# Kernel tuning notes

Measured on AMD Instinct MI355X. Metric: run time of the kernel, lower is better.

The kernel has to match this reference:

```python
import jax, jax.numpy as jnp
import numpy as np

N = 12288
IN_DIM = 128
OUT_DIM = 128
LR_SLOPE = 0.01
NEG_INF = -9e16


def setup_inputs() -> dict:
    key = jax.random.key(0)
    k1, k2, k3, k4 = jax.random.split(key, 4)
    emb_mat = jax.random.normal(k1, (N, IN_DIM), dtype=jnp.float32)
    adj_mat = jax.random.randint(k2, (N, N), 0, 2, dtype=jnp.int32)
    # xavier-normal-ish init for params
    W = jax.random.normal(k3, (OUT_DIM, IN_DIM), dtype=jnp.float32) * (2.0 / (IN_DIM + OUT_DIM)) ** 0.5
    a = jax.random.normal(k4, (2 * OUT_DIM, 1), dtype=jnp.float32) * (2.0 / (2 * OUT_DIM + 1)) ** 0.5
    return {"emb_mat": emb_mat, "adj_mat": adj_mat, "W": W, "a": a}


def reference(emb_mat, adj_mat, W, a):
    out_dim = W.shape[0]
    e_new = emb_mat @ W.T                       # [N, D_out]
    a1 = a[:out_dim, :]                         # [D_out, 1]
    a2 = a[out_dim:, :]                         # [D_out, 1]
    source_scores = e_new @ a1                  # [N, 1]
    target_scores = e_new @ a2                  # [N, 1]
    e = source_scores + target_scores.T         # [N, N] outer sum
    e = jax.nn.leaky_relu(e, negative_slope=LR_SLOPE)
    e = jnp.where(adj_mat > 0, e, NEG_INF)
    attention = jax.nn.softmax(e, axis=-1)      # [N, N]
    e_transf = attention @ e_new                # [N, D_out]
    return jax.nn.relu(e_transf)
```

## Files before the change

### kernel.cpp

```cpp
#include <hip/hip_runtime.h>


#define NN 12288
#define DIM 128
#define CSPLIT 8
#define COLS_PER (NN / CSPLIT)
#define BK 32
#define NCHUNK (COLS_PER / BK)
#define LOG2E 1.4426950408889634f

typedef __bf16 bf16x8 __attribute__((ext_vector_type(8)));
typedef float f32x4 __attribute__((ext_vector_type(4)));

__device__ __forceinline__ void gl_lds16(const __bf16* g, __bf16* l) {
  __builtin_amdgcn_global_load_lds(
      (const __attribute__((address_space(1))) void*)g,
      (__attribute__((address_space(3))) void*)l, 16, 0, 0);
}

__global__ __launch_bounds__(256) void k1_gemm(const float* __restrict__ emb,
                                               const float* __restrict__ W,
                                               const float* __restrict__ a,
                                               __bf16* __restrict__ Vt,
                                               float* __restrict__ s,
                                               float* __restrict__ t) {
  const int lane = threadIdx.x & 63;
  const int wave = threadIdx.x >> 6;
  const int m = lane & 15;
  const int quad = lane >> 4;
  const int row0 = blockIdx.x * 64 + wave * 16;

  f32x4 acc[8];
#pragma unroll
  for (int nb = 0; nb < 8; nb++) acc[nb] = (f32x4){0.f, 0.f, 0.f, 0.f};

#pragma unroll
  for (int ks = 0; ks < 4; ks++) {
    const int k0 = ks * 32 + quad * 8;
    const float* ep = emb + (size_t)(row0 + m) * DIM + k0;
    float4 lo = *(const float4*)ep;
    float4 hi = *(const float4*)(ep + 4);
    bf16x8 af = {(__bf16)lo.x, (__bf16)lo.y, (__bf16)lo.z, (__bf16)lo.w,
                 (__bf16)hi.x, (__bf16)hi.y, (__bf16)hi.z, (__bf16)hi.w};
#pragma unroll
    for (int nb = 0; nb < 8; nb++) {
      const float* wp = W + (size_t)(nb * 16 + m) * DIM + k0;
      float4 wlo = *(const float4*)wp;
      float4 whi = *(const float4*)(wp + 4);
      bf16x8 bf = {(__bf16)wlo.x, (__bf16)wlo.y, (__bf16)wlo.z, (__bf16)wlo.w,
                   (__bf16)whi.x, (__bf16)whi.y, (__bf16)whi.z, (__bf16)whi.w};
      acc[nb] = __builtin_amdgcn_mfma_f32_16x16x32_bf16(af, bf, acc[nb], 0, 0, 0);
    }
  }

  float a1v[8], a2v[8];
#pragma unroll
  for (int nb = 0; nb < 8; nb++) {
    a1v[nb] = a[nb * 16 + m];
    a2v[nb] = a[DIM + nb * 16 + m];
  }
#pragma unroll
  for (int r = 0; r < 4; r++) {
    const int gr = row0 + quad * 4 + r;
    float ps = 0.f, pt = 0.f;
#pragma unroll
    for (int nb = 0; nb < 8; nb++) {
      float e = acc[nb][r];
      ps += e * a1v[nb];
      pt += e * a2v[nb];
      Vt[(size_t)(nb * 16 + m) * NN + gr] = (__bf16)e;
    }
    ps += __shfl_xor(ps, 1); ps += __shfl_xor(ps, 2);
    ps += __shfl_xor(ps, 4); ps += __shfl_xor(ps, 8);
    pt += __shfl_xor(pt, 1); pt += __shfl_xor(pt, 2);
    pt += __shfl_xor(pt, 4); pt += __shfl_xor(pt, 8);
    if (m == 0) { s[gr] = ps * LOG2E; t[gr] = pt * LOG2E; }
  }
}

__global__ __launch_bounds__(256) void ktmax(const float* __restrict__ t,
                                             float* __restrict__ tmax) {
  __shared__ float red[4];
  const float4* t4 = (const float4*)t;
  float mx = -3.0e38f;
#pragma unroll
  for (int i = 0; i < NN / 4 / 256; i++) {
    float4 v = t4[i * 256 + threadIdx.x];
    mx = fmaxf(mx, fmaxf(fmaxf(v.x, v.y), fmaxf(v.z, v.w)));
  }
#pragma unroll
  for (int off = 1; off < 64; off <<= 1) mx = fmaxf(mx, __shfl_xor(mx, off));
  if ((threadIdx.x & 63) == 0) red[threadIdx.x >> 6] = mx;
  __syncthreads();
  if (threadIdx.x == 0)
    *tmax = fmaxf(fmaxf(red[0], red[1]), fmaxf(red[2], red[3]));
}

#define PELS(P, AA0, AA1, T0, T1, SS, MM, LL)                                   \
  {                                                                             \
    float v0 = SS + T0.x, v1 = SS + T0.y, v2 = SS + T0.z, v3 = SS + T0.w;       \
    float v4 = SS + T1.x, v5 = SS + T1.y, v6 = SS + T1.z, v7 = SS + T1.w;       \
    float e0 = (AA0.x != 0) ? __builtin_amdgcn_exp2f(fmaxf(v0, 0.01f * v0) - MM) : 0.f; \
    float e1 = (AA0.y != 0) ? __builtin_amdgcn_exp2f(fmaxf(v1, 0.01f * v1) - MM) : 0.f; \
    float e2 = (AA0.z != 0) ? __builtin_amdgcn_exp2f(fmaxf(v2, 0.01f * v2) - MM) : 0.f; \
    float e3 = (AA0.w != 0) ? __builtin_amdgcn_exp2f(fmaxf(v3, 0.01f * v3) - MM) : 0.f; \
    float e4 = (AA1.x != 0) ? __builtin_amdgcn_exp2f(fmaxf(v4, 0.01f * v4) - MM) : 0.f; \
    float e5 = (AA1.y != 0) ? __builtin_amdgcn_exp2f(fmaxf(v5, 0.01f * v5) - MM) : 0.f; \
    float e6 = (AA1.z != 0) ? __builtin_amdgcn_exp2f(fmaxf(v6, 0.01f * v6) - MM) : 0.f; \
    float e7 = (AA1.w != 0) ? __builtin_amdgcn_exp2f(fmaxf(v7, 0.01f * v7) - MM) : 0.f; \
    LL += ((e0 + e1) + (e2 + e3)) + ((e4 + e5) + (e6 + e7));                    \
    P[0] = (__bf16)e0; P[1] = (__bf16)e1; P[2] = (__bf16)e2; P[3] = (__bf16)e3; \
    P[4] = (__bf16)e4; P[5] = (__bf16)e5; P[6] = (__bf16)e6; P[7] = (__bf16)e7; \
  }

#define FETCH(cc, A0A, A1A, A0B, A1B, T0, T1)                                   \
  {                                                                             \
    const int off = (cc) * BK;                                                  \
    A0A = *(const int4*)(abase + off); A1A = *(const int4*)(abase + off + 4);   \
    A0B = *(const int4*)(bbase + off); A1B = *(const int4*)(bbase + off + 4);   \
    T0 = *(const float4*)(tbase + off); T1 = *(const float4*)(tbase + off + 4); \
  }

#define DMA2(cc)                                                                \
  {                                                                             \
    __bf16* d = &vtb[(cc) & 3][dst0];                                           \
    gl_lds16(vsrc0 + (size_t)(cc) * BK, d);                                     \
    gl_lds16(vsrc1 + (size_t)(cc) * BK, d + 512);                               \
  }

#define COMPUTE(cc, A0A, A1A, A0B, A1B, T0, T1)                                 \
  {                                                                             \
    const __bf16* vb = &vtb[(cc) & 3][vread];                                   \
    bf16x8 pA, pB;                                                              \
    PELS(pA, A0A, A1A, T0, T1, sA, mA, lA)                                      \
    PELS(pB, A0B, A1B, T0, T1, sB, mB, lB)                                      \
    _Pragma("unroll")                                                           \
    for (int nb = 0; nb < 8; nb++) {                                            \
      bf16x8 bv = *(const bf16x8*)(vb + nb * 512);                              \
      accA[nb] = __builtin_amdgcn_mfma_f32_16x16x32_bf16(pA, bv, accA[nb], 0, 0, 0); \
      accB[nb] = __builtin_amdgcn_mfma_f32_16x16x32_bf16(pB, bv, accB[nb], 0, 0, 0); \
    }                                                                           \
  }

__global__ __launch_bounds__(256, 3) void k2_attn(const int* __restrict__ adj,
                                                  const __bf16* __restrict__ Vt,
                                                  const float* __restrict__ sK,
                                                  const float* __restrict__ tK,
                                                  const float* __restrict__ tmaxp,
                                                  float* __restrict__ part,
                                                  float* __restrict__ lpart) {
  __shared__ __attribute__((aligned(16))) __bf16 vtb[4][4096];

  const int tid = threadIdx.x;
  const int lane = tid & 63;
  const int wave = tid >> 6;
  const int m = lane & 15;
  const int quad = lane >> 4;
  const int row0 = blockIdx.x * 128;
  const int cs = blockIdx.y;
  const int col0 = cs * COLS_PER;
  const int rowA = row0 + wave * 32 + m;
  const int rowB = rowA + 16;

  const float TmaxK = *tmaxp;
  const float sA = sK[rowA], sB = sK[rowB];
  const float uA = sA + TmaxK, uB = sB + TmaxK;
  const float mA = fmaxf(uA, 0.01f * uA);
  const float mB = fmaxf(uB, 0.01f * uB);

  const int p0 = wave * 128 + lane;
  const int r0d = p0 >> 2;
  const int cg0 = (p0 & 3) ^ ((r0d >> 1) & 3);
  const __bf16* vsrc0 = Vt + (size_t)r0d * NN + col0 + cg0 * 8;
  const __bf16* vsrc1 = vsrc0 + (size_t)16 * NN;
  const int dst0 = wave * 1024;
  const int vread = (m * 4 + (quad ^ ((m >> 1) & 3))) * 8;

  const int* abase = adj + (size_t)rowA * NN + col0 + quad * 8;
  const int* bbase = adj + (size_t)rowB * NN + col0 + quad * 8;
  const float* tbase = tK + col0 + quad * 8;

  f32x4 accA[8], accB[8];
#pragma unroll
  for (int nb = 0; nb < 8; nb++) {
    accA[nb] = (f32x4){0.f, 0.f, 0.f, 0.f};
    accB[nb] = (f32x4){0.f, 0.f, 0.f, 0.f};
  }
  float lA = 0.f, lB = 0.f;

  int4 xA0, xA1, xB0, xB1; float4 xT0, xT1;
  int4 yA0, yA1, yB0, yB1; float4 yT0, yT1;

  DMA2(0);
  DMA2(1);
  FETCH(0, xA0, xA1, xB0, xB1, xT0, xT1);
  asm volatile("s_waitcnt vmcnt(0)" ::: "memory");
  __builtin_amdgcn_s_barrier();

  for (int c = 0; c < NCHUNK; c += 2) {
    if (c + 2 < NCHUNK) DMA2(c + 2);
    FETCH(c + 1, yA0, yA1, yB0, yB1, yT0, yT1);
    COMPUTE(c, xA0, xA1, xB0, xB1, xT0, xT1);
    asm volatile("s_waitcnt vmcnt(4)" ::: "memory");
    __builtin_amdgcn_s_barrier();

    if (c + 3 < NCHUNK) DMA2(c + 3);
    if (c + 2 < NCHUNK) FETCH(c + 2, xA0, xA1, xB0, xB1, xT0, xT1);
    COMPUTE(c + 1, yA0, yA1, yB0, yB1, yT0, yT1);
    if (c + 2 < NCHUNK) {
      asm volatile("s_waitcnt vmcnt(4)" ::: "memory");
      __builtin_amdgcn_s_barrier();
    }
  }

  lA += __shfl_xor(lA, 16); lA += __shfl_xor(lA, 32);
  lB += __shfl_xor(lB, 16); lB += __shfl_xor(lB, 32);
  if (quad == 0) {
    lpart[(size_t)cs * NN + rowA] = lA;
    lpart[(size_t)cs * NN + rowB] = lB;
  }

  float* po = part + ((size_t)cs * NN + row0 + wave * 32) * DIM;
#pragma unroll
  for (int nb = 0; nb < 8; nb++) {
#pragma unroll
    for (int r = 0; r < 4; r++) {
      po[(size_t)(quad * 4 + r) * DIM + nb * 16 + m] = accA[nb][r];
      po[(size_t)(16 + quad * 4 + r) * DIM + nb * 16 + m] = accB[nb][r];
    }
  }
}

__global__ __launch_bounds__(256) void k3_fin(const float* __restrict__ part,
                                              const float* __restrict__ lpart,
                                              float* __restrict__ out) {
  __shared__ float li[8];
  const int base = blockIdx.x * 256;
  const int idx = base + (int)threadIdx.x;
  if (threadIdx.x < 8) {
    const int r = (base >> 5) + (int)threadIdx.x;
    float l = 0.f;
#pragma unroll
    for (int c2 = 0; c2 < CSPLIT; c2++) l += lpart[(size_t)c2 * NN + r];
    li[threadIdx.x] = 1.0f / l;
  }
  const float4* p4 = (const float4*)part;
  float4 acc = p4[idx];
#pragma unroll
  for (int c2 = 1; c2 < CSPLIT; c2++) {
    float4 v = p4[(size_t)c2 * (NN * DIM / 4) + idx];
    acc.x += v.x; acc.y += v.y; acc.z += v.z; acc.w += v.w;
  }
  __syncthreads();
  const float liv = li[threadIdx.x >> 5];
  float4 o;
  o.x = fmaxf(acc.x * liv, 0.f);
  o.y = fmaxf(acc.y * liv, 0.f);
  o.z = fmaxf(acc.z * liv, 0.f);
  o.w = fmaxf(acc.w * liv, 0.f);
  ((float4*)out)[idx] = o;
}

extern "C" void kernel_launch(void* const* d_in, const int* in_sizes, int n_in,
                              void* d_out, int out_size, void* d_ws, size_t ws_size,
                              hipStream_t stream) {
  (void)in_sizes; (void)n_in; (void)out_size; (void)ws_size;
  const float* emb = (const float*)d_in[0];
  const int* adj = (const int*)d_in[1];
  const float* W = (const float*)d_in[2];
  const float* a = (const float*)d_in[3];
  float* out = (float*)d_out;

  char* ws = (char*)d_ws;
  __bf16* Vt = (__bf16*)ws;
  float* s = (float*)(ws + 3145728);
  float* t = (float*)(ws + 3194880);
  float* lpart = (float*)(ws + 3244032);
  float* tmax = (float*)(ws + 3686400);
  float* part = (float*)(ws + 3686656);

  k1_gemm<<<NN / 64, 256, 0, stream>>>(emb, W, a, Vt, s, t);
  ktmax<<<1, 256, 0, stream>>>(t, tmax);
  dim3 g2(NN / 128, CSPLIT);
  k2_attn<<<g2, 256, 0, stream>>>(adj, Vt, s, t, tmax, part, lpart);
  k3_fin<<<NN * DIM / 4 / 256, 256, 0, stream>>>(part, lpart, out);
}
```

Baseline: 832.8 us.

## Load V operand directly from global memory instead of staging through LDS

Removes the LDS staging of the transposed V tiles (global_load_lds DMA, swizzled layout, barriers) and has each wave read its bf16 V fragments straight from global/L2 inside the MFMA loop. The t-score loads move into the compute step. The grid is flattened to 1D with the column split as the fastest index, so blocks sharing a column slice of V run close together and can hit in cache. This removes barrier and LDS overhead and the 3-block occupancy hint, but adds redundant per-wave global loads of V with long stride and makes latency hiding depend on the compiler.

After: 957.9 us. 15.0% more time.

```diff
diff --git a/kernel.cpp b/kernel.cpp
--- a/kernel.cpp
+++ b/kernel.cpp
@@ -11,12 +11,6 @@
 
 typedef __bf16 bf16x8 __attribute__((ext_vector_type(8)));
 typedef float f32x4 __attribute__((ext_vector_type(4)));
-
-__device__ __forceinline__ void gl_lds16(const __bf16* g, __bf16* l) {
-  __builtin_amdgcn_global_load_lds(
-      (const __attribute__((address_space(1))) void*)g,
-      (__attribute__((address_space(3))) void*)l, 16, 0, 0);
-}
 
 __global__ __launch_bounds__(256) void k1_gemm(const float* __restrict__ emb,
                                                const float* __restrict__ W,
@@ -113,51 +107,46 @@
     P[4] = (__bf16)e4; P[5] = (__bf16)e5; P[6] = (__bf16)e6; P[7] = (__bf16)e7; \
   }
 
-#define FETCH(cc, A0A, A1A, A0B, A1B, T0, T1)                                   \
+#define FETCH(cc, A0A, A1A, A0B, A1B)                                           \
   {                                                                             \
     const int off = (cc) * BK;                                                  \
     A0A = *(const int4*)(abase + off); A1A = *(const int4*)(abase + off + 4);   \
     A0B = *(const int4*)(bbase + off); A1B = *(const int4*)(bbase + off + 4);   \
-    T0 = *(const float4*)(tbase + off); T1 = *(const float4*)(tbase + off + 4); \
-  }
-
-#define DMA2(cc)                                                                \
+  }
+
+#define COMPUTE(cc, A0A, A1A, A0B, A1B)                                         \
   {                                                                             \
-    __bf16* d = &vtb[(cc) & 3][dst0];                                           \
-    gl_lds16(vsrc0 + (size_t)(cc) * BK, d);                                     \
-    gl_lds16(vsrc1 + (size_t)(cc) * BK, d + 512);                               \
-  }
-
-#define COMPUTE(cc, A0A, A1A, A0B, A1B, T0, T1)                                 \
-  {                                                                             \
-    const __bf16* vb = &vtb[(cc) & 3][vread];                                   \
+    const float* tp = tbase + (cc) * BK;                                        \
+    float4 t0 = *(const float4*)tp;                                             \
+    float4 t1 = *(const float4*)(tp + 4);                                       \
+    const __bf16* vp = vbase + (cc) * BK;                                       \
     bf16x8 pA, pB;                                                              \
-    PELS(pA, A0A, A1A, T0, T1, sA, mA, lA)                                      \
-    PELS(pB, A0B, A1B, T0, T1, sB, mB, lB)                                      \
+    PELS(pA, A0A, A1A, t0, t1, sA, mA, lA)                                      \
+    PELS(pB, A0B, A1B, t0, t1, sB, mB, lB)                                      \
     _Pragma("unroll")                                                           \
     for (int nb = 0; nb < 8; nb++) {                                            \
-      bf16x8 bv = *(const bf16x8*)(vb + nb * 512);                              \
+      bf16x8 bv = *(const bf16x8*)(vp + (size_t)(nb * 16) * NN);                \
       accA[nb] = __builtin_amdgcn_mfma_f32_16x16x32_bf16(pA, bv, accA[nb], 0, 0, 0); \
       accB[nb] = __builtin_amdgcn_mfma_f32_16x16x32_bf16(pB, bv, accB[nb], 0, 0, 0); \
     }                                                                           \
   }
 
-__global__ __launch_bounds__(256, 3) void k2_attn(const int* __restrict__ adj,
-                                                  const __bf16* __restrict__ Vt,
-                                                  const float* __restrict__ sK,
-                                                  const float* __restrict__ tK,
-                                                  const float* __restrict__ tmaxp,
-                                                  float* __restrict__ part,
-                                                  float* __restrict__ lpart) {
-  __shared__ __attribute__((aligned(16))) __bf16 vtb[4][4096];
-
+__global__ __launch_bounds__(256) void k2_attn(const int* __restrict__ adj,
+                                               const __bf16* __restrict__ Vt,
+                                               const float* __restrict__ sK,
+                                               const float* __restrict__ tK,
+                                               const float* __restrict__ tmaxp,
+                                               float* __restrict__ part,
+                                               float* __restrict__ lpart) {
   const int tid = threadIdx.x;
   const int lane = tid & 63;
   const int wave = tid >> 6;
   const int m = lane & 15;
   const int quad = lane >> 4;
-  const int row0 = blockIdx.x * 128;
-  const int cs = blockIdx.y;
+  const int bid = blockIdx.x;
+  const int cs = bid & 7;
+  const int xb = bid >> 3;
+  const int row0 = xb * 128;
   const int col0 = cs * COLS_PER;
   const int rowA = row0 + wave * 32 + m;
   const int rowB = rowA + 16;
@@ -168,17 +157,10 @@
   const float mA = fmaxf(uA, 0.01f * uA);
   const float mB = fmaxf(uB, 0.01f * uB);
 
-  const int p0 = wave * 128 + lane;
-  const int r0d = p0 >> 2;
-  const int cg0 = (p0 & 3) ^ ((r0d >> 1) & 3);
-  const __bf16* vsrc0 = Vt + (size_t)r0d * NN + col0 + cg0 * 8;
-  const __bf16* vsrc1 = vsrc0 + (size_t)16 * NN;
-  const int dst0 = wave * 1024;
-  const int vread = (m * 4 + (quad ^ ((m >> 1) & 3))) * 8;
-
   const int* abase = adj + (size_t)rowA * NN + col0 + quad * 8;
   const int* bbase = adj + (size_t)rowB * NN + col0 + quad * 8;
   const float* tbase = tK + col0 + quad * 8;
+  const __bf16* vbase = Vt + (size_t)m * NN + col0 + quad * 8;
 
   f32x4 accA[8], accB[8];
 #pragma unroll
@@ -188,29 +170,16 @@
   }
   float lA = 0.f, lB = 0.f;
 
-  int4 xA0, xA1, xB0, xB1; float4 xT0, xT1;
-  int4 yA0, yA1, yB0, yB1; float4 yT0, yT1;
-
-  DMA2(0);
-  DMA2(1);
-  FETCH(0, xA0, xA1, xB0, xB1, xT0, xT1);
-  asm volatile("s_waitcnt vmcnt(0)" ::: "memory");
-  __builtin_amdgcn_s_barrier();
+  int4 xA0, xA1, xB0, xB1;
+  int4 yA0, yA1, yB0, yB1;
+
+  FETCH(0, xA0, xA1, xB0, xB1);
 
   for (int c = 0; c < NCHUNK; c += 2) {
-    if (c + 2 < NCHUNK) DMA2(c + 2);
-    FETCH(c + 1, yA0, yA1, yB0, yB1, yT0, yT1);
-    COMPUTE(c, xA0, xA1, xB0, xB1, xT0, xT1);
-    asm volatile("s_waitcnt vmcnt(4)" ::: "memory");
-    __builtin_amdgcn_s_barrier();
-
-    if (c + 3 < NCHUNK) DMA2(c + 3);
-    if (c + 2 < NCHUNK) FETCH(c + 2, xA0, xA1, xB0, xB1, xT0, xT1);
-    COMPUTE(c + 1, yA0, yA1, yB0, yB1, yT0, yT1);
-    if (c + 2 < NCHUNK) {
-      asm volatile("s_waitcnt vmcnt(4)" ::: "memory");
-      __builtin_amdgcn_s_barrier();
-    }
+    FETCH(c + 1, yA0, yA1, yB0, yB1);
+    COMPUTE(c, xA0, xA1, xB0, xB1);
+    if (c + 2 < NCHUNK) FETCH(c + 2, xA0, xA1, xB0, xB1);
+    COMPUTE(c + 1, yA0, yA1, yB0, yB1);
   }
 
   lA += __shfl_xor(lA, 16); lA += __shfl_xor(lA, 32);
@@ -281,7 +250,6 @@
 
   k1_gemm<<<NN / 64, 256, 0, stream>>>(emb, W, a, Vt, s, t);
   ktmax<<<1, 256, 0, stream>>>(t, tmax);
-  dim3 g2(NN / 128, CSPLIT);
-  k2_attn<<<g2, 256, 0, stream>>>(adj, Vt, s, t, tmax, part, lpart);
+  k2_attn<<<NN / 128 * CSPLIT, 256, 0, stream>>>(adj, Vt, s, t, tmax, part, lpart);
   k3_fin<<<NN * DIM / 4 / 256, 256, 0, stream>>>(part, lpart, out);
 }
```

## Pack adjacency into bitmask in a pre-pass and read bits in attention kernel

Applied to the files above, without the earlier changes.

Adds a streaming kernel that converts the int32 adjacency matrix into a 1-bit-per-entry mask using wave ballots and bit interleaving. The attention kernel then reads one 32-bit word per row chunk instead of 32 int32 values, which shrinks the loads it must overlap with MFMA work. The full adjacency read still happens, now in a separate pass with an extra launch and workspace buffer. The attention grid is also flattened so the column splits of a row block are launched adjacently.

New measurement: 891.0 us. 1.07x slower.

```diff
diff --git a/kernel.cpp b/kernel.cpp
--- a/kernel.cpp
+++ b/kernel.cpp
@@ -7,6 +7,7 @@
 #define COLS_PER (NN / CSPLIT)
 #define BK 32
 #define NCHUNK (COLS_PER / BK)
+#define NWPR (NN / 32)
 #define LOG2E 1.4426950408889634f
 
 typedef __bf16 bf16x8 __attribute__((ext_vector_type(8)));
@@ -16,6 +17,38 @@
   __builtin_amdgcn_global_load_lds(
       (const __attribute__((address_space(1))) void*)g,
       (__attribute__((address_space(3))) void*)l, 16, 0, 0);
+}
+
+__device__ __forceinline__ unsigned spread4(unsigned b) {
+  b = (b | (b << 12)) & 0x000F000Fu;
+  b = (b | (b << 6))  & 0x03030303u;
+  b = (b | (b << 3))  & 0x11111111u;
+  return b;
+}
+
+#define PACK_BLOCKS 2048
+#define PACK_ITERS (NN * (NN / 32) / (PACK_BLOCKS * 4) / 8)
+
+__global__ __launch_bounds__(256) void kpack(const int* __restrict__ adj,
+                                             unsigned* __restrict__ adjP) {
+  const int lane = threadIdx.x & 63;
+  const int gw = blockIdx.x * 4 + (threadIdx.x >> 6);
+#pragma unroll 4
+  for (int it = 0; it < PACK_ITERS; it++) {
+    const size_t wb = ((size_t)gw * PACK_ITERS + it) * 8;
+    int4 v = *(const int4*)(adj + wb * 32 + lane * 4);
+    unsigned long long bx = __ballot(v.x != 0);
+    unsigned long long by = __ballot(v.y != 0);
+    unsigned long long bz = __ballot(v.z != 0);
+    unsigned long long bw = __ballot(v.w != 0);
+    if (lane < 8) {
+      unsigned sx = spread4((unsigned)(bx >> (lane * 8)) & 0xFFu);
+      unsigned sy = spread4((unsigned)(by >> (lane * 8)) & 0xFFu);
+      unsigned sz = spread4((unsigned)(bz >> (lane * 8)) & 0xFFu);
+      unsigned sw = spread4((unsigned)(bw >> (lane * 8)) & 0xFFu);
+      adjP[wb + lane] = sx | (sy << 1) | (sz << 2) | (sw << 3);
+    }
+  }
 }
 
 __global__ __launch_bounds__(256) void k1_gemm(const float* __restrict__ emb,
@@ -96,29 +129,21 @@
     *tmax = fmaxf(fmaxf(red[0], red[1]), fmaxf(red[2], red[3]));
 }
 
-#define PELS(P, AA0, AA1, T0, T1, SS, MM, LL)                                   \
+#define PELS(P, WQ, T0, T1, SS, MM, LL)                                         \
   {                                                                             \
     float v0 = SS + T0.x, v1 = SS + T0.y, v2 = SS + T0.z, v3 = SS + T0.w;       \
     float v4 = SS + T1.x, v5 = SS + T1.y, v6 = SS + T1.z, v7 = SS + T1.w;       \
-    float e0 = (AA0.x != 0) ? __builtin_amdgcn_exp2f(fmaxf(v0, 0.01f * v0) - MM) : 0.f; \
-    float e1 = (AA0.y != 0) ? __builtin_amdgcn_exp2f(fmaxf(v1, 0.01f * v1) - MM) : 0.f; \
-    float e2 = (AA0.z != 0) ? __builtin_amdgcn_exp2f(fmaxf(v2, 0.01f * v2) - MM) : 0.f; \
-    float e3 = (AA0.w != 0) ? __builtin_amdgcn_exp2f(fmaxf(v3, 0.01f * v3) - MM) : 0.f; \
-    float e4 = (AA1.x != 0) ? __builtin_amdgcn_exp2f(fmaxf(v4, 0.01f * v4) - MM) : 0.f; \
-    float e5 = (AA1.y != 0) ? __builtin_amdgcn_exp2f(fmaxf(v5, 0.01f * v5) - MM) : 0.f; \
-    float e6 = (AA1.z != 0) ? __builtin_amdgcn_exp2f(fmaxf(v6, 0.01f * v6) - MM) : 0.f; \
-    float e7 = (AA1.w != 0) ? __builtin_amdgcn_exp2f(fmaxf(v7, 0.01f * v7) - MM) : 0.f; \
+    float e0 = ((WQ) & 1u)        ? __builtin_amdgcn_exp2f(fmaxf(v0, 0.01f * v0) - MM) : 0.f; \
+    float e1 = ((WQ >> 1) & 1u)   ? __builtin_amdgcn_exp2f(fmaxf(v1, 0.01f * v1) - MM) : 0.f; \
+    float e2 = ((WQ >> 2) & 1u)   ? __builtin_amdgcn_exp2f(fmaxf(v2, 0.01f * v2) - MM) : 0.f; \
+    float e3 = ((WQ >> 3) & 1u)   ? __builtin_amdgcn_exp2f(fmaxf(v3, 0.01f * v3) - MM) : 0.f; \
+    float e4 = ((WQ >> 4) & 1u)   ? __builtin_amdgcn_exp2f(fmaxf(v4, 0.01f * v4) - MM) : 0.f; \
+    float e5 = ((WQ >> 5) & 1u)   ? __builtin_amdgcn_exp2f(fmaxf(v5, 0.01f * v5) - MM) : 0.f; \
+    float e6 = ((WQ >> 6) & 1u)   ? __builtin_amdgcn_exp2f(fmaxf(v6, 0.01f * v6) - MM) : 0.f; \
+    float e7 = ((WQ >> 7) & 1u)   ? __builtin_amdgcn_exp2f(fmaxf(v7, 0.01f * v7) - MM) : 0.f; \
     LL += ((e0 + e1) + (e2 + e3)) + ((e4 + e5) + (e6 + e7));                    \
     P[0] = (__bf16)e0; P[1] = (__bf16)e1; P[2] = (__bf16)e2; P[3] = (__bf16)e3; \
     P[4] = (__bf16)e4; P[5] = (__bf16)e5; P[6] = (__bf16)e6; P[7] = (__bf16)e7; \
-  }
-
-#define FETCH(cc, A0A, A1A, A0B, A1B, T0, T1)                                   \
-  {                                                                             \
-    const int off = (cc) * BK;                                                  \
-    A0A = *(const int4*)(abase + off); A1A = *(const int4*)(abase + off + 4);   \
-    A0B = *(const int4*)(bbase + off); A1B = *(const int4*)(bbase + off + 4);   \
-    T0 = *(const float4*)(tbase + off); T1 = *(const float4*)(tbase + off + 4); \
   }
 
 #define DMA2(cc)                                                                \
@@ -128,12 +153,22 @@
     gl_lds16(vsrc1 + (size_t)(cc) * BK, d + 512);                               \
   }
 
-#define COMPUTE(cc, A0A, A1A, A0B, A1B, T0, T1)                                 \
+#define FETCHP(cc, WA, WB, T0, T1)                                              \
   {                                                                             \
+    WA = apA[(cc)];                                                             \
+    WB = apB[(cc)];                                                             \
+    const float* tp = tbase + (cc) * BK;                                        \
+    T0 = *(const float4*)tp;  T1 = *(const float4*)(tp + 4);                    \
+  }
+
+#define COMPC(cc, WA, WB, T0, T1)                                               \
+  {                                                                             \
+    const unsigned wqA = (WA) >> qsh;                                           \
+    const unsigned wqB = (WB) >> qsh;                                           \
     const __bf16* vb = &vtb[(cc) & 3][vread];                                   \
     bf16x8 pA, pB;                                                              \
-    PELS(pA, A0A, A1A, T0, T1, sA, mA, lA)                                      \
-    PELS(pB, A0B, A1B, T0, T1, sB, mB, lB)                                      \
+    PELS(pA, wqA, T0, T1, sA, mA, lA)                                           \
+    PELS(pB, wqB, T0, T1, sB, mB, lB)                                           \
     _Pragma("unroll")                                                           \
     for (int nb = 0; nb < 8; nb++) {                                            \
       bf16x8 bv = *(const bf16x8*)(vb + nb * 512);                              \
@@ -142,7 +177,9 @@
     }                                                                           \
   }
 
-__global__ __launch_bounds__(256, 3) void k2_attn(const int* __restrict__ adj,
+#define WAIT6 { asm volatile("s_waitcnt vmcnt(6)" ::: "memory"); __builtin_amdgcn_s_barrier(); }
+
+__global__ __launch_bounds__(256, 3) void k2_attn(const unsigned* __restrict__ adjP,
                                                   const __bf16* __restrict__ Vt,
                                                   const float* __restrict__ sK,
                                                   const float* __restrict__ tK,
@@ -156,8 +193,11 @@
   const int wave = tid >> 6;
   const int m = lane & 15;
   const int quad = lane >> 4;
-  const int row0 = blockIdx.x * 128;
-  const int cs = blockIdx.y;
+  const int qsh = quad * 8;
+  const int bid = blockIdx.x;
+  const int cs = bid & 7;
+  const int xb = bid >> 3;
+  const int row0 = xb * 128;
   const int col0 = cs * COLS_PER;
   const int rowA = row0 + wave * 32 + m;
   const int rowB = rowA + 16;
@@ -176,8 +216,8 @@
   const int dst0 = wave * 1024;
   const int vread = (m * 4 + (quad ^ ((m >> 1) & 3))) * 8;
 
-  const int* abase = adj + (size_t)rowA * NN + col0 + quad * 8;
-  const int* bbase = adj + (size_t)rowB * NN + col0 + quad * 8;
+  const unsigned* apA = adjP + (size_t)rowA * NWPR + cs * (COLS_PER / 32);
+  const unsigned* apB = adjP + (size_t)rowB * NWPR + cs * (COLS_PER / 32);
   const float* tbase = tK + col0 + quad * 8;
 
   f32x4 accA[8], accB[8];
@@ -188,29 +228,23 @@
   }
   float lA = 0.f, lB = 0.f;
 
-  int4 xA0, xA1, xB0, xB1; float4 xT0, xT1;
-  int4 yA0, yA1, yB0, yB1; float4 yT0, yT1;
-
-  DMA2(0);
-  DMA2(1);
-  FETCH(0, xA0, xA1, xB0, xB1, xT0, xT1);
-  asm volatile("s_waitcnt vmcnt(0)" ::: "memory");
-  __builtin_amdgcn_s_barrier();
+  unsigned wXa, wXb, wYa, wYb;
+  float4 tX0, tX1, tY0, tY1;
+
+  DMA2(0); DMA2(1);
+  FETCHP(0, wXa, wXb, tX0, tX1);
+  WAIT6;
 
   for (int c = 0; c < NCHUNK; c += 2) {
     if (c + 2 < NCHUNK) DMA2(c + 2);
-    FETCH(c + 1, yA0, yA1, yB0, yB1, yT0, yT1);
-    COMPUTE(c, xA0, xA1, xB0, xB1, xT0, xT1);
-    asm volatile("s_waitcnt vmcnt(4)" ::: "memory");
-    __builtin_amdgcn_s_barrier();
+    FETCHP(c + 1, wYa, wYb, tY0, tY1);
+    COMPC(c, wXa, wXb, tX0, tX1);
+    WAIT6;
 
     if (c + 3 < NCHUNK) DMA2(c + 3);
-    if (c + 2 < NCHUNK) FETCH(c + 2, xA0, xA1, xB0, xB1, xT0, xT1);
-    COMPUTE(c + 1, yA0, yA1, yB0, yB1, yT0, yT1);
-    if (c + 2 < NCHUNK) {
-      asm volatile("s_waitcnt vmcnt(4)" ::: "memory");
-      __builtin_amdgcn_s_barrier();
-    }
+    if (c + 2 < NCHUNK) FETCHP(c + 2, wXa, wXb, tX0, tX1);
+    COMPC(c + 1, wYa, wYb, tY0, tY1);
+    if (c + 2 < NCHUNK) WAIT6;
   }
 
   lA += __shfl_xor(lA, 16); lA += __shfl_xor(lA, 32);
@@ -278,10 +312,11 @@
   float* lpart = (float*)(ws + 3244032);
   float* tmax = (float*)(ws + 3686400);
   float* part = (float*)(ws + 3686656);
-
+  unsigned* adjP = (unsigned*)(ws + 54018304);
+
+  kpack<<<PACK_BLOCKS, 256, 0, stream>>>(adj, adjP);
   k1_gemm<<<NN / 64, 256, 0, stream>>>(emb, W, a, Vt, s, t);
   ktmax<<<1, 256, 0, stream>>>(t, tmax);
-  dim3 g2(NN / 128, CSPLIT);
-  k2_attn<<<g2, 256, 0, stream>>>(adj, Vt, s, t, tmax, part, lpart);
+  k2_attn<<<NN / 128 * CSPLIT, 256, 0, stream>>>(adjP, Vt, s, t, tmax, part, lpart);
   k3_fin<<<NN * DIM / 4 / 256, 256, 0, stream>>>(part, lpart, out);
 }
```
